# Optimization experiments

Hardware: AMD Instinct MI355X
Metric: run time of the kernel (lower is better)

Reference implementation:

```python
import jax, jax.numpy as jnp
import numpy as np

IN_F = 2048
OUT_F = 2048
BS = 64  # block_size
NIB = IN_F // BS   # 32 in-blocks
NOB = OUT_F // BS  # 32 out-blocks


def setup_inputs() -> dict:
    key = jax.random.key(0)
    k_x, k_s1, k_s2, k_m = jax.random.split(key, 4)
    bound = 1.0 / np.sqrt(BS)
    x = jax.random.normal(k_x, (4, 4096, IN_F), dtype=jnp.float32)
    stage1 = jax.random.uniform(k_s1, (NIB * BS, BS), minval=-bound, maxval=bound, dtype=jnp.float32)
    stage2 = jax.random.uniform(k_s2, (NOB * BS, BS), minval=-bound, maxval=bound, dtype=jnp.float32)
    mix_w = jax.random.normal(k_m, (NOB * BS, NIB * BS), dtype=jnp.float32) / np.sqrt(IN_F)
    return {"x": x, "stage1": stage1, "stage2": stage2, "mix_w": mix_w}


def _blockdiag(x, weight, num_blocks):
    # x: [..., num_blocks*BS]; weight: [num_blocks*BS, BS] viewed as [g, c, d]
    shape = x.shape[:-1]
    xg = x.reshape(-1, num_blocks, BS)
    w = weight.reshape(num_blocks, BS, BS)
    y = jnp.einsum('ngc,gcd->ngd', xg, w)
    return y.reshape(*shape, num_blocks * BS)


def _shuffle(x):
    # interpret last dim as [BS, NIB], transpose to [NIB, BS]
    shape = x.shape[:-1]
    return x.reshape(-1, BS, NIB).transpose(0, 2, 1).reshape(*shape, NIB * BS)


def reference(x, stage1, stage2, mix_w):
    h = _blockdiag(x, stage1, NIB)          # [B,S,IN_F]
    h = _shuffle(h)                          # [B,S,IN_F]
    h = jnp.einsum('bsi,oi->bso', h, mix_w)  # dense mix, no bias
    return _blockdiag(h, stage2, NOB)        # [B,S,OUT_F]
```

## Files before the change

kernel.cpp:

```cpp
#include <hip/hip_runtime.h>
#include <stdint.h>

#define IN_F 2048
#define OUT_F 2048
#define MTOK 16384

typedef __attribute__((ext_vector_type(8))) __bf16 bf16x8;
typedef __attribute__((ext_vector_type(4))) float f32x4;
typedef __attribute__((ext_vector_type(4))) unsigned short us4;

typedef const __attribute__((address_space(1))) void g_void;
typedef __attribute__((address_space(3))) void l_void;

__device__ __forceinline__ void async16(void* lds, const void* g) {
    __builtin_amdgcn_global_load_lds((g_void*)(uintptr_t)g, (l_void*)(uintptr_t)lds, 16, 0, 0);
}

__device__ __forceinline__ unsigned short f2bf(float x) {
    union { float f; uint32_t u; } v; v.f = x;
    uint32_t r = v.u + 0x7fffu + ((v.u >> 16) & 1u);
    return (unsigned short)(r >> 16);
}

#define FP 68

__global__ __launch_bounds__(256) void k_fold_conv(
    const float* __restrict__ X, const float* __restrict__ s1,
    const float* __restrict__ s2, const float* __restrict__ MW,
    unsigned short* __restrict__ Xb, unsigned short* __restrict__ Bb) {
    __shared__ float lds[3 * 64 * FP];
    const int t = threadIdx.x;
    const int bx = blockIdx.x;

    if (bx >= 1024) {
        const int gid = (bx - 1024) * 256 + t;
        const float4* src = (const float4*)X;
        us4* dst = (us4*)Xb;
#pragma unroll
        for (int k = 0; k < 16; ++k) {
            int idx = k * (2048 * 256) + gid;
            float4 v = src[idx];
            us4 o;
            o[0] = f2bf(v.x); o[1] = f2bf(v.y); o[2] = f2bf(v.z); o[3] = f2bf(v.w);
            dst[idx] = o;
        }
        return;
    }

    float* Wl  = lds;
    float* Bpl = lds + 64 * FP;
    float* M1t = lds + 128 * FP;
    const int g  = bx & 31;
    const int rt = bx >> 5;

#pragma unroll
    for (int q = 0; q < 4; ++q) {
        int id = q * 256 + t;
        int c = id >> 4, d4 = id & 15;
        float4 v = *(const float4*)(s1 + (size_t)(g * 64 + c) * 64 + d4 * 4);
        *(float4*)&Wl[c * FP + d4 * 4] = v;
    }
#pragma unroll
    for (int q = 0; q < 8; ++q) {
        int id = q * 256 + t;
        int o = id >> 5, b = id & 31;
        float2 v = *(const float2*)(MW + (size_t)(rt * 64 + o) * 2048 + b * 64 + g * 2);
        Bpl[o * FP + b]      = v.x;
        Bpl[o * FP + b + 32] = v.y;
    }
    __syncthreads();

    {
        const int co = (t & 15) * 4, oo = (t >> 4) * 4;
        float acc[4][4] = {};
#pragma unroll
        for (int dc = 0; dc < 16; ++dc) {
            float4 bv[4], wv[4];
#pragma unroll
            for (int i = 0; i < 4; ++i) bv[i] = *(const float4*)&Bpl[(oo + i) * FP + dc * 4];
#pragma unroll
            for (int j = 0; j < 4; ++j) wv[j] = *(const float4*)&Wl[(co + j) * FP + dc * 4];
#pragma unroll
            for (int i = 0; i < 4; ++i)
#pragma unroll
                for (int j = 0; j < 4; ++j)
                    acc[i][j] += bv[i].x * wv[j].x + bv[i].y * wv[j].y
                               + bv[i].z * wv[j].z + bv[i].w * wv[j].w;
        }
#pragma unroll
        for (int i = 0; i < 4; ++i)
#pragma unroll
            for (int j = 0; j < 4; ++j)
                M1t[(co + j) * FP + oo + i] = acc[i][j];
    }
    __syncthreads();

#pragma unroll
    for (int q = 0; q < 16; ++q) {
        int id = q * 256 + t;
        int d2 = id & 63, c2 = id >> 6;
        Wl[d2 * FP + c2] = s2[(size_t)(rt * 64 + c2) * 64 + d2];
    }
    __syncthreads();

    {
        const int cco = (t & 15) * 4, d2o = (t >> 4) * 4;
        float acc[4][4] = {};
#pragma unroll
        for (int kc = 0; kc < 16; ++kc) {
            float4 wv[4], mv[4];
#pragma unroll
            for (int i = 0; i < 4; ++i) wv[i] = *(const float4*)&Wl[(d2o + i) * FP + kc * 4];
#pragma unroll
            for (int j = 0; j < 4; ++j) mv[j] = *(const float4*)&M1t[(cco + j) * FP + kc * 4];
#pragma unroll
            for (int i = 0; i < 4; ++i)
#pragma unroll
                for (int j = 0; j < 4; ++j)
                    acc[i][j] += wv[i].x * mv[j].x + wv[i].y * mv[j].y
                               + wv[i].z * mv[j].z + wv[i].w * mv[j].w;
        }
#pragma unroll
        for (int i = 0; i < 4; ++i) {
            us4 o;
            o[0] = f2bf(acc[i][0]); o[1] = f2bf(acc[i][1]);
            o[2] = f2bf(acc[i][2]); o[3] = f2bf(acc[i][3]);
            *(us4*)(Bb + (size_t)(rt * 64 + d2o + i) * 2048 + g * 64 + cco) = o;
        }
    }
}

__global__ __launch_bounds__(256, 2) void k_gemm(
    const unsigned short* __restrict__ A, const unsigned short* __restrict__ B,
    float* __restrict__ C) {
    __shared__ unsigned short smem[16384];
    unsigned short* As = smem;
    unsigned short* Bs = smem + 8192;
    const int t = threadIdx.x;
    const int lane = t & 63, wave = t >> 6;
    const int quad = lane >> 4, l16 = lane & 15;
    const int mw = wave & 1, nw = wave >> 1;
    const int lin = blockIdx.y * 128 + blockIdx.x;
    const int m0 = (lin >> 4) * 128;
    const int n0 = (lin & 15) * 128;
    const int rr = t >> 3, chunk = t & 7;
    const int gsw = (chunk ^ (rr & 7)) * 8;
    const int lsw = l16 & 7;

    f32x4 acc[4][4];
#pragma unroll
    for (int i = 0; i < 4; ++i)
#pragma unroll
        for (int j = 0; j < 4; ++j) acc[i][j] = (f32x4)0.f;

    for (int kb = 0; kb < IN_F; kb += 64) {
#pragma unroll
        for (int q = 0; q < 4; ++q) {
            int r = q * 32 + rr;
            async16((char*)As + (size_t)(q * 4096 + t * 16),
                    A + (size_t)(m0 + r) * IN_F + kb + gsw);
            async16((char*)Bs + (size_t)(q * 4096 + t * 16),
                    B + (size_t)(n0 + r) * IN_F + kb + gsw);
        }
        __syncthreads();
#pragma unroll
        for (int ks = 0; ks < 2; ++ks) {
            bf16x8 af[4], bfr[4];
#pragma unroll
            for (int i = 0; i < 4; ++i)
                af[i] = *(const bf16x8*)(As + (mw * 64 + i * 16 + l16) * 64
                                            + (((ks * 4 + quad) ^ lsw) * 8));
#pragma unroll
            for (int j = 0; j < 4; ++j)
                bfr[j] = *(const bf16x8*)(Bs + (nw * 64 + j * 16 + l16) * 64
                                             + (((ks * 4 + quad) ^ lsw) * 8));
#pragma unroll
            for (int i = 0; i < 4; ++i)
#pragma unroll
                for (int j = 0; j < 4; ++j)
                    acc[i][j] = __builtin_amdgcn_mfma_f32_16x16x32_bf16(af[i], bfr[j], acc[i][j], 0, 0, 0);
        }
        __syncthreads();
    }

#pragma unroll
    for (int i = 0; i < 4; ++i)
#pragma unroll
        for (int j = 0; j < 4; ++j) {
            float* Cp = C + (size_t)(m0 + mw * 64 + i * 16 + quad * 4) * OUT_F
                          + (n0 + nw * 64 + j * 16 + l16);
#pragma unroll
            for (int r = 0; r < 4; ++r) Cp[(size_t)r * OUT_F] = acc[i][j][r];
        }
}

extern "C" void kernel_launch(void* const* d_in, const int* in_sizes, int n_in,
                              void* d_out, int out_size, void* d_ws, size_t ws_size,
                              hipStream_t stream) {
    const float* x  = (const float*)d_in[0];
    const float* s1 = (const float*)d_in[1];
    const float* s2 = (const float*)d_in[2];
    const float* mw = (const float*)d_in[3];
    float* out = (float*)d_out;

    char* ws = (char*)d_ws;
    unsigned short* Xb = (unsigned short*)ws;
    unsigned short* Bb = (unsigned short*)(ws + (size_t)MTOK * IN_F * 2);

    k_fold_conv<<<3072, 256, 0, stream>>>(x, s1, s2, mw, Xb, Bb);
    k_gemm<<<dim3(128, 16), 256, 0, stream>>>(Xb, Bb, out);
}
```

Before: 468.3 us.

## Split fold/convert kernels, reduce fold LDS, skew LDS reads, remap GEMM blocks for XCDs

The fused fold+convert kernel is split into two kernels. The fold kernel now uses two LDS buffers instead of three, loads s2 with float4 instead of scalar transposed stores, and rotates the k index per lane to spread LDS bank accesses. The GEMM block index is remapped so consecutive blocks map to tiles spread across XCDs, aiming at better L2 locality. The risks are an extra kernel launch and different dispatch overlap.

Result: faster. 419.0 us (-10.5%).

```diff
diff --git a/kernel.cpp b/kernel.cpp
--- a/kernel.cpp
+++ b/kernel.cpp
@@ -22,64 +22,65 @@
     return (unsigned short)(r >> 16);
 }
 
+__global__ __launch_bounds__(256) void k_convert(
+    const float* __restrict__ X, unsigned short* __restrict__ Xb) {
+    const int gid = blockIdx.x * 256 + threadIdx.x;
+    const float4* src = (const float4*)X;
+    us4* dst = (us4*)Xb;
+#pragma unroll
+    for (int k = 0; k < 16; ++k) {
+        int idx = k * (2048 * 256) + gid;
+        float4 v = src[idx];
+        us4 o;
+        o[0] = f2bf(v.x); o[1] = f2bf(v.y); o[2] = f2bf(v.z); o[3] = f2bf(v.w);
+        dst[idx] = o;
+    }
+}
+
 #define FP 68
 
-__global__ __launch_bounds__(256) void k_fold_conv(
-    const float* __restrict__ X, const float* __restrict__ s1,
-    const float* __restrict__ s2, const float* __restrict__ MW,
-    unsigned short* __restrict__ Xb, unsigned short* __restrict__ Bb) {
-    __shared__ float lds[3 * 64 * FP];
+__global__ __launch_bounds__(256) void k_fold(
+    const float* __restrict__ s1, const float* __restrict__ s2,
+    const float* __restrict__ MW, unsigned short* __restrict__ Bb) {
+    __shared__ float B0[64 * FP];
+    __shared__ float B1[64 * FP];
     const int t = threadIdx.x;
-    const int bx = blockIdx.x;
-
-    if (bx >= 1024) {
-        const int gid = (bx - 1024) * 256 + t;
-        const float4* src = (const float4*)X;
-        us4* dst = (us4*)Xb;
-#pragma unroll
-        for (int k = 0; k < 16; ++k) {
-            int idx = k * (2048 * 256) + gid;
-            float4 v = src[idx];
-            us4 o;
-            o[0] = f2bf(v.x); o[1] = f2bf(v.y); o[2] = f2bf(v.z); o[3] = f2bf(v.w);
-            dst[idx] = o;
-        }
-        return;
-    }
-
-    float* Wl  = lds;
-    float* Bpl = lds + 64 * FP;
-    float* M1t = lds + 128 * FP;
-    const int g  = bx & 31;
-    const int rt = bx >> 5;
+    const int g  = blockIdx.x & 31;
+    const int rt = blockIdx.x >> 5;
+    const int l = t & 15, h = t >> 4;
 
 #pragma unroll
     for (int q = 0; q < 4; ++q) {
         int id = q * 256 + t;
         int c = id >> 4, d4 = id & 15;
-        float4 v = *(const float4*)(s1 + (size_t)(g * 64 + c) * 64 + d4 * 4);
-        *(float4*)&Wl[c * FP + d4 * 4] = v;
+        *(float4*)&B0[c * FP + d4 * 4] =
+            *(const float4*)(s1 + (size_t)(g * 64 + c) * 64 + d4 * 4);
     }
 #pragma unroll
     for (int q = 0; q < 8; ++q) {
         int id = q * 256 + t;
         int o = id >> 5, b = id & 31;
         float2 v = *(const float2*)(MW + (size_t)(rt * 64 + o) * 2048 + b * 64 + g * 2);
-        Bpl[o * FP + b]      = v.x;
-        Bpl[o * FP + b + 32] = v.y;
+        B1[o * FP + b]      = v.x;
+        B1[o * FP + b + 32] = v.y;
     }
     __syncthreads();
 
+    float acc[4][4];
+#pragma unroll
+    for (int i = 0; i < 4; ++i)
+#pragma unroll
+        for (int j = 0; j < 4; ++j) acc[i][j] = 0.f;
     {
-        const int co = (t & 15) * 4, oo = (t >> 4) * 4;
-        float acc[4][4] = {};
+        const int co = l * 4, oo = h * 4;
 #pragma unroll
         for (int dc = 0; dc < 16; ++dc) {
+            const int dce = (dc + l) & 15;
             float4 bv[4], wv[4];
 #pragma unroll
-            for (int i = 0; i < 4; ++i) bv[i] = *(const float4*)&Bpl[(oo + i) * FP + dc * 4];
-#pragma unroll
-            for (int j = 0; j < 4; ++j) wv[j] = *(const float4*)&Wl[(co + j) * FP + dc * 4];
+            for (int i = 0; i < 4; ++i) bv[i] = *(const float4*)&B1[(oo + i) * FP + dce * 4];
+#pragma unroll
+            for (int j = 0; j < 4; ++j) wv[j] = *(const float4*)&B0[(co + j) * FP + dce * 4];
 #pragma unroll
             for (int i = 0; i < 4; ++i)
 #pragma unroll
@@ -87,38 +88,46 @@
                     acc[i][j] += bv[i].x * wv[j].x + bv[i].y * wv[j].y
                                + bv[i].z * wv[j].z + bv[i].w * wv[j].w;
         }
+    }
+    __syncthreads();
+
+    {
+        const int co = l * 4, oo = h * 4;
+#pragma unroll
+        for (int j = 0; j < 4; ++j) {
+            float4 v; v.x = acc[0][j]; v.y = acc[1][j]; v.z = acc[2][j]; v.w = acc[3][j];
+            *(float4*)&B0[(co + j) * FP + oo] = v;
+        }
+    }
+#pragma unroll
+    for (int q = 0; q < 4; ++q) {
+        int id = q * 256 + t;
+        int c2 = id >> 4, d4 = id & 15;
+        *(float4*)&B1[c2 * FP + d4 * 4] =
+            *(const float4*)(s2 + (size_t)(rt * 64 + c2) * 64 + d4 * 4);
+    }
+    __syncthreads();
+
+    {
+        const int d2o = l * 4, cco = h * 4;
 #pragma unroll
         for (int i = 0; i < 4; ++i)
 #pragma unroll
-            for (int j = 0; j < 4; ++j)
-                M1t[(co + j) * FP + oo + i] = acc[i][j];
-    }
-    __syncthreads();
-
-#pragma unroll
-    for (int q = 0; q < 16; ++q) {
-        int id = q * 256 + t;
-        int d2 = id & 63, c2 = id >> 6;
-        Wl[d2 * FP + c2] = s2[(size_t)(rt * 64 + c2) * 64 + d2];
-    }
-    __syncthreads();
-
-    {
-        const int cco = (t & 15) * 4, d2o = (t >> 4) * 4;
-        float acc[4][4] = {};
+            for (int j = 0; j < 4; ++j) acc[i][j] = 0.f;
 #pragma unroll
         for (int kc = 0; kc < 16; ++kc) {
-            float4 wv[4], mv[4];
-#pragma unroll
-            for (int i = 0; i < 4; ++i) wv[i] = *(const float4*)&Wl[(d2o + i) * FP + kc * 4];
-#pragma unroll
-            for (int j = 0; j < 4; ++j) mv[j] = *(const float4*)&M1t[(cco + j) * FP + kc * 4];
+            const int kce = (kc + l) & 15;
+            float4 wv4[4], mv[4];
+#pragma unroll
+            for (int s = 0; s < 4; ++s) wv4[s] = *(const float4*)&B1[(kce * 4 + s) * FP + d2o];
+#pragma unroll
+            for (int j = 0; j < 4; ++j) mv[j] = *(const float4*)&B0[(cco + j) * FP + kce * 4];
 #pragma unroll
             for (int i = 0; i < 4; ++i)
 #pragma unroll
                 for (int j = 0; j < 4; ++j)
-                    acc[i][j] += wv[i].x * mv[j].x + wv[i].y * mv[j].y
-                               + wv[i].z * mv[j].z + wv[i].w * mv[j].w;
+                    acc[i][j] += wv4[0][i] * mv[j].x + wv4[1][i] * mv[j].y
+                               + wv4[2][i] * mv[j].z + wv4[3][i] * mv[j].w;
         }
 #pragma unroll
         for (int i = 0; i < 4; ++i) {
@@ -140,7 +149,8 @@
     const int lane = t & 63, wave = t >> 6;
     const int quad = lane >> 4, l16 = lane & 15;
     const int mw = wave & 1, nw = wave >> 1;
-    const int lin = blockIdx.y * 128 + blockIdx.x;
+    const int orig = blockIdx.y * 128 + blockIdx.x;
+    const int lin = (orig & 7) * 256 + (orig >> 3);
     const int m0 = (lin >> 4) * 128;
     const int n0 = (lin & 15) * 128;
     const int rr = t >> 3, chunk = t & 7;
@@ -207,6 +217,7 @@
     unsigned short* Xb = (unsigned short*)ws;
     unsigned short* Bb = (unsigned short*)(ws + (size_t)MTOK * IN_F * 2);
 
-    k_fold_conv<<<3072, 256, 0, stream>>>(x, s1, s2, mw, Xb, Bb);
+    k_fold<<<1024, 256, 0, stream>>>(s1, s2, mw, Bb);
+    k_convert<<<2048, 256, 0, stream>>>(x, Xb);
     k_gemm<<<dim3(128, 16), 256, 0, stream>>>(Xb, Bb, out);
 }
```
